# Optimization experiments

Hardware: AMD Instinct MI355X
Metric: run time of the kernel (lower is better)

## Reference

```python
import jax, jax.numpy as jnp
import numpy as np

N = 30000   # nodes
E = 600000  # edges
IN = 256    # in_channels
HID = 128   # 2*out_channels
OUT = 64    # out_channels


def setup_inputs() -> dict:
    key = jax.random.key(0)
    k = jax.random.split(key, 6)
    x = jax.random.normal(k[0], (N, IN), dtype=jnp.float32)
    edge_index = jax.random.randint(k[1], (2, E), 0, N, dtype=jnp.int64)
    W1 = jax.random.normal(k[2], (IN, HID), dtype=jnp.float32) * (1.0 / np.sqrt(IN))
    b1 = jnp.zeros((HID,), dtype=jnp.float32)
    W2 = jax.random.normal(k[3], (HID, OUT), dtype=jnp.float32) * (1.0 / np.sqrt(HID))
    b2 = jnp.zeros((OUT,), dtype=jnp.float32)
    return {"x": x, "edge_index": edge_index, "W1": W1, "b1": b1, "W2": W2, "b2": b2}


def _gcn_norm(edge_index, n_nodes):
    # PyG gcn_norm with add_self_loops=True, edge_weight=1
    loop = jnp.arange(n_nodes, dtype=edge_index.dtype)
    src = jnp.concatenate([edge_index[0], loop])
    dst = jnp.concatenate([edge_index[1], loop])
    deg = jax.ops.segment_sum(jnp.ones_like(dst, dtype=jnp.float32), dst,
                              num_segments=n_nodes)
    dinv = jnp.where(deg > 0, jax.lax.rsqrt(deg), 0.0)
    norm = dinv[src] * dinv[dst]  # [E+N]
    return src, dst, norm


def _gcn_conv(h, src, dst, norm, W, b, n_nodes):
    h = h @ W                              # [N, out] linear first (PyG order)
    msg = h[src] * norm[:, None]           # gather + per-edge scale, [E+N, out]
    out = jax.ops.segment_sum(msg, dst, num_segments=n_nodes)  # scatter-add
    return out + b


def reference(x, edge_index, W1, b1, W2, b2):
    n_nodes = x.shape[0]
    src, dst, norm = _gcn_norm(edge_index, n_nodes)
    h = _gcn_conv(x, src, dst, norm, W1, b1, n_nodes)
    h = jax.nn.relu(h)
    return _gcn_conv(h, src, dst, norm, W2, b2, n_nodes)
```

## Files before the change

### kernel.cpp

```cpp
#include <hip/hip_runtime.h>


#define GCN_IN 256
#define GCN_HID 128
#define GCN_OUT 64

#define BKT 128
#define SBE 4096
#define CAP 4096
#define SRCM 0x1FFFFFFu

typedef unsigned short ushort_t;
typedef __attribute__((ext_vector_type(8))) short short8;
typedef __attribute__((ext_vector_type(8))) unsigned short ushort8;
typedef __attribute__((ext_vector_type(4))) float f32x4;

__device__ inline float bf2f(ushort_t u) {
  union { unsigned int i; float f; } x; x.i = ((unsigned int)u) << 16; return x.f;
}
__device__ inline ushort_t f2bf(float f) {
  union { float f; unsigned int i; } u; u.f = f;
  unsigned int r = u.i + 0x7FFFu + ((u.i >> 16) & 1u);
  return (ushort_t)(r >> 16);
}

__global__ __launch_bounds__(256)
void stageX_kernel(const int* __restrict__ ei, int E,
                   int* __restrict__ gcur, int nbin,
                   unsigned int* __restrict__ stage) {
  __shared__ int lcnt[256];
  __shared__ int cur[256];
  __shared__ int nzc;
  const int t = threadIdx.x;
  const int sb = blockIdx.x;
  lcnt[t] = 0;
  if (t == 0) nzc = 0;
  __syncthreads();
  if (t < 128 && ei[2 * t + 1] != 0) atomicAdd(&nzc, 1);
  __syncthreads();
  const bool i64 = (nzc == 0);
  const int base = sb * SBE;
  int end = base + SBE; if (end > E) end = E;

  unsigned int p[16];
  int bk[16];
#pragma unroll
  for (int k = 0; k < 16; ++k) {
    int i = base + t + k * 256;
    bk[k] = -1;
    if (i < end) {
      int s, d;
      if (i64) { s = ei[2 * i]; d = ei[2 * E + 2 * i]; }
      else     { s = ei[i];     d = ei[E + i]; }
      p[k] = (unsigned int)s | ((unsigned int)(d & 127) << 25);
      bk[k] = d >> 7;
      atomicAdd(&lcnt[bk[k]], 1);
    }
  }
  __syncthreads();
  for (int b = t; b < nbin; b += 256) {
    int c = lcnt[b];
    cur[b] = b * CAP + (c ? atomicAdd(&gcur[b], c) : 0);
  }
  __syncthreads();
#pragma unroll
  for (int k = 0; k < 16; ++k) {
    if (bk[k] >= 0) {
      int pos = atomicAdd(&cur[bk[k]], 1);
      if (pos < (bk[k] + 1) * CAP)
        stage[pos] = p[k];
    }
  }
}

__global__ __launch_bounds__(256)
void scatter_kernel(const unsigned int* __restrict__ stage,
                    const int* __restrict__ gcur, int nbin,
                    int* __restrict__ csr_src,
                    int* __restrict__ row_ptr, int* __restrict__ deg,
                    float* __restrict__ dinv, int n) {
  __shared__ int lcnt[BKT];
  __shared__ int lscan[BKT];
  __shared__ int lcur[BKT];
  const int t = threadIdx.x;
  const int b = blockIdx.x;
  const int node0 = b * BKT;
  const int nn = (n - node0 < BKT) ? (n - node0) : BKT;
  const int rb = b * CAP;
  const int re = rb + gcur[b];
  if (t < BKT) lcnt[t] = 0;
  __syncthreads();
  for (int i = rb + t; i < re; i += 256)
    atomicAdd(&lcnt[stage[i] >> 25], 1);
  __syncthreads();
  if (t < BKT) lscan[t] = lcnt[t];
  __syncthreads();
  for (int off = 1; off < BKT; off <<= 1) {
    int v = 0;
    if (t < BKT && t >= off) v = lscan[t - off];
    __syncthreads();
    if (t < BKT) lscan[t] += v;
    __syncthreads();
  }
  if (t < BKT) {
    int excl = rb + lscan[t] - lcnt[t];
    lcur[t] = excl;
    if (t < nn) {
      row_ptr[node0 + t] = excl;
      deg[node0 + t] = lcnt[t];
      dinv[node0 + t] = rsqrtf((float)(lcnt[t] + 1));
    }
  }
  __syncthreads();
  for (int i = rb + t; i < re; i += 256) {
    unsigned int p = stage[i];
    int l = p >> 25;
    int pos = atomicAdd(&lcur[l], 1);
    csr_src[pos] = (int)(p & SRCM);
  }
}

__global__ void prep_w_kernel(const void* __restrict__ W1, const void* __restrict__ W2,
                              ushort_t* __restrict__ Wt1, ushort_t* __restrict__ Wt2,
                              int* __restrict__ flags, int* __restrict__ gcur) {
  __shared__ int csh;
  if (threadIdx.x == 0) csh = 0;
  __syncthreads();
  if (threadIdx.x < 128) {
    ushort_t u = ((const ushort_t*)W1)[2 * threadIdx.x];
    int e = (u >> 7) & 0xFF;
    if (e >= 100 && e <= 140) atomicAdd(&csh, 1);
  }
  __syncthreads();
  bool f32 = (csh < 64);
  if (blockIdx.x == 0) {
    if (threadIdx.x == 0) flags[0] = f32 ? 1 : 0;
    gcur[threadIdx.x] = 0;
  }

  int i = blockIdx.x * blockDim.x + threadIdx.x;
  if (i < GCN_IN * GCN_HID) {
    int k = i >> 7, n = i & 127;
    float v = f32 ? ((const float*)W1)[i] : bf2f(((const ushort_t*)W1)[i]);
    Wt1[n * GCN_IN + k] = f2bf(v);
  }
  int j = i - GCN_IN * GCN_HID;
  if (j >= 0 && j < GCN_HID * GCN_OUT) {
    int k = j >> 6, n = j & 63;
    float v = f32 ? ((const float*)W2)[j] : bf2f(((const ushort_t*)W2)[j]);
    Wt2[n * GCN_HID + k] = f2bf(v);
  }
}

template<int K, int NC, int A_MODE>
__global__ __launch_bounds__(256)
void gemm_mfma_kernel(const void* __restrict__ A, const ushort_t* __restrict__ Bt,
                      ushort_t* __restrict__ C, int M, const int* __restrict__ flags) {
  constexpr int KH = (K > 128) ? 128 : K;
  constexpr int KPC = KH / 8;
  constexpr int NT = NC / 32;
  __shared__ ushort_t As[32 * KH];
  __shared__ ushort_t Bs[NC * KH];
  const int tid = threadIdx.x;
  const int wv = tid >> 6;
  const int lane = tid & 63;
  const int ml = lane & 15;
  const int quad = lane >> 4;
  const int row0 = blockIdx.x * 32;
  const int mrow = (wv & 1) * 16 + ml;
  const int ncol0 = (wv >> 1) * (NC / 2);
  const bool aF32 = (A_MODE == 0) && (flags[0] != 0);
  f32x4 acc[NT] = {};

  for (int ch = 0; ch < K; ch += KH) {
    if (ch) __syncthreads();
    for (int c = tid; c < 32 * KPC; c += 256) {
      int r = c / KPC, cq = c % KPC;
      ushort8 o;
      if (row0 + r < M) {
        if (aF32) {
          const float* ap = (const float*)A + (size_t)(row0 + r) * K + ch + cq * 8;
          float4 f0 = *(const float4*)ap;
          float4 f1 = *(const float4*)(ap + 4);
          o[0] = f2bf(f0.x); o[1] = f2bf(f0.y); o[2] = f2bf(f0.z); o[3] = f2bf(f0.w);
          o[4] = f2bf(f1.x); o[5] = f2bf(f1.y); o[6] = f2bf(f1.z); o[7] = f2bf(f1.w);
        } else {
          o = *(const ushort8*)((const ushort_t*)A + (size_t)(row0 + r) * K + ch + cq * 8);
        }
      } else {
        o = (ushort8)0;
      }
      int byte = (cq * 16) ^ ((r & 7) << 4);
      *(ushort8*)((char*)As + r * (KH * 2) + byte) = o;
    }
    for (int c = tid; c < NC * KPC; c += 256) {
      int nr = c / KPC, cq = c % KPC;
      ushort8 o = *(const ushort8*)(Bt + (size_t)nr * K + ch + cq * 8);
      int byte = (cq * 16) ^ ((nr & 7) << 4);
      *(ushort8*)((char*)Bs + nr * (KH * 2) + byte) = o;
    }
    __syncthreads();
#pragma unroll
    for (int kt = 0; kt < KH; kt += 32) {
      int abyte = (kt * 2 + quad * 16) ^ ((mrow & 7) << 4);
      short8 af = *(const short8*)((const char*)As + mrow * (KH * 2) + abyte);
#pragma unroll
      for (int t = 0; t < NT; ++t) {
        int nr = ncol0 + t * 16 + ml;
        int bbyte = (kt * 2 + quad * 16) ^ ((nr & 7) << 4);
        short8 bf = *(const short8*)((const char*)Bs + nr * (KH * 2) + bbyte);
        acc[t] = __builtin_amdgcn_mfma_f32_16x16x32_bf16(af, bf, acc[t], 0, 0, 0);
      }
    }
  }

  const int orow = row0 + (wv & 1) * 16 + quad * 4;
#pragma unroll
  for (int t = 0; t < NT; ++t) {
    int col = ncol0 + t * 16 + ml;
#pragma unroll
    for (int r = 0; r < 4; ++r) {
      if (orow + r < M)
        C[(size_t)(orow + r) * NC + col] = f2bf(acc[t][r]);
    }
  }
}


__global__ void aggregate_relu_kernel(const ushort_t* __restrict__ h,
                                      const int* __restrict__ row_ptr,
                                      const int* __restrict__ deg,
                                      const int* __restrict__ csr_src,
                                      const float* __restrict__ dinv,
                                      const void* __restrict__ bias,
                                      ushort_t* __restrict__ outp, int n,
                                      const int* __restrict__ flags) {
  int wave = threadIdx.x >> 6;
  int lane = threadIdx.x & 63;
  int v = blockIdx.x * (blockDim.x >> 6) + wave;
  if (v >= n) return;
  const int q = lane & 15, g = lane >> 4;
  float acc[8] = {};
  int beg = row_ptr[v], end = beg + deg[v];
  for (int base = beg; base < end; base += 64) {
    int navail = end - base; if (navail > 64) navail = 64;
    int sv = 0; float dv = 0.f;
    if (base + lane < end) { sv = csr_src[base + lane]; dv = dinv[sv]; }
    for (int j = 0; j < navail; j += 16) {
      int e0 = j + g, e1 = j + 4 + g, e2 = j + 8 + g, e3 = j + 12 + g;
      int s0 = __shfl(sv, e0), s1 = __shfl(sv, e1);
      int s2 = __shfl(sv, e2), s3 = __shfl(sv, e3);
      float d0 = __shfl(dv, e0), d1 = __shfl(dv, e1);
      float d2 = __shfl(dv, e2), d3 = __shfl(dv, e3);
      ushort8 hv0 = *(const ushort8*)(h + (size_t)s0 * GCN_HID + q * 8);
      ushort8 hv1 = *(const ushort8*)(h + (size_t)s1 * GCN_HID + q * 8);
      ushort8 hv2 = *(const ushort8*)(h + (size_t)s2 * GCN_HID + q * 8);
      ushort8 hv3 = *(const ushort8*)(h + (size_t)s3 * GCN_HID + q * 8);
#pragma unroll
      for (int k = 0; k < 8; ++k) {
        acc[k] = fmaf(d0, bf2f(hv0[k]), acc[k]);
        acc[k] = fmaf(d1, bf2f(hv1[k]), acc[k]);
        acc[k] = fmaf(d2, bf2f(hv2[k]), acc[k]);
        acc[k] = fmaf(d3, bf2f(hv3[k]), acc[k]);
      }
    }
  }
#pragma unroll
  for (int k = 0; k < 8; ++k) {
    acc[k] += __shfl_xor(acc[k], 16);
    acc[k] += __shfl_xor(acc[k], 32);
  }
  if (g == 0) {
    float di = dinv[v];
    float sl = di * di;
    ushort8 hv = *(const ushort8*)(h + (size_t)v * GCN_HID + q * 8);
    const bool bF32 = flags[0] != 0;
    ushort8 o;
#pragma unroll
    for (int k = 0; k < 8; ++k) {
      float bv = bF32 ? ((const float*)bias)[q * 8 + k]
                      : bf2f(((const ushort_t*)bias)[q * 8 + k]);
      o[k] = f2bf(fmaxf(di * acc[k] + sl * bf2f(hv[k]) + bv, 0.f));
    }
    *(ushort8*)(outp + (size_t)v * GCN_HID + q * 8) = o;
  }
}

__global__ void aggregate_out_kernel(const ushort_t* __restrict__ h,
                                     const int* __restrict__ row_ptr,
                                     const int* __restrict__ deg,
                                     const int* __restrict__ csr_src,
                                     const float* __restrict__ dinv,
                                     const void* __restrict__ bias,
                                     void* __restrict__ outp, int n,
                                     const int* __restrict__ flags) {
  int wave = threadIdx.x >> 6;
  int lane = threadIdx.x & 63;
  int v = blockIdx.x * (blockDim.x >> 6) + wave;
  if (v >= n) return;
  const int q = lane & 7, g = lane >> 3;
  float acc[8] = {};
  int beg = row_ptr[v], end = beg + deg[v];
  for (int base = beg; base < end; base += 64) {
    int navail = end - base; if (navail > 64) navail = 64;
    int sv = 0; float dv = 0.f;
    if (base + lane < end) { sv = csr_src[base + lane]; dv = dinv[sv]; }
    for (int j = 0; j < navail; j += 32) {
      int e0 = j + g, e1 = j + 8 + g, e2 = j + 16 + g, e3 = j + 24 + g;
      int s0 = __shfl(sv, e0), s1 = __shfl(sv, e1);
      int s2 = __shfl(sv, e2), s3 = __shfl(sv, e3);
      float d0 = __shfl(dv, e0), d1 = __shfl(dv, e1);
      float d2 = __shfl(dv, e2), d3 = __shfl(dv, e3);
      ushort8 hv0 = *(const ushort8*)(h + (size_t)s0 * GCN_OUT + q * 8);
      ushort8 hv1 = *(const ushort8*)(h + (size_t)s1 * GCN_OUT + q * 8);
      ushort8 hv2 = *(const ushort8*)(h + (size_t)s2 * GCN_OUT + q * 8);
      ushort8 hv3 = *(const ushort8*)(h + (size_t)s3 * GCN_OUT + q * 8);
#pragma unroll
      for (int k = 0; k < 8; ++k) {
        acc[k] = fmaf(d0, bf2f(hv0[k]), acc[k]);
        acc[k] = fmaf(d1, bf2f(hv1[k]), acc[k]);
        acc[k] = fmaf(d2, bf2f(hv2[k]), acc[k]);
        acc[k] = fmaf(d3, bf2f(hv3[k]), acc[k]);
      }
    }
  }
#pragma unroll
  for (int k = 0; k < 8; ++k) {
    acc[k] += __shfl_xor(acc[k], 8);
    acc[k] += __shfl_xor(acc[k], 16);
    acc[k] += __shfl_xor(acc[k], 32);
  }
  if (g == 0) {
    float di = dinv[v];
    float sl = di * di;
    ushort8 hv = *(const ushort8*)(h + (size_t)v * GCN_OUT + q * 8);
    const bool oF32 = flags[0] != 0;
    float r[8];
#pragma unroll
    for (int k = 0; k < 8; ++k) {
      float bv = oF32 ? ((const float*)bias)[q * 8 + k]
                      : bf2f(((const ushort_t*)bias)[q * 8 + k]);
      r[k] = di * acc[k] + sl * bf2f(hv[k]) + bv;
    }
    if (oF32) {
      float* op = (float*)outp + (size_t)v * GCN_OUT + q * 8;
      *(float4*)op = make_float4(r[0], r[1], r[2], r[3]);
      *(float4*)(op + 4) = make_float4(r[4], r[5], r[6], r[7]);
    } else {
      ushort8 o;
#pragma unroll
      for (int k = 0; k < 8; ++k) o[k] = f2bf(r[k]);
      *(ushort8*)((ushort_t*)outp + (size_t)v * GCN_OUT + q * 8) = o;
    }
  }
}


extern "C" void kernel_launch(void* const* d_in, const int* in_sizes, int n_in,
                              void* d_out, int out_size, void* d_ws, size_t ws_size,
                              hipStream_t stream) {
  const void* x  = d_in[0];
  const int*  ei = (const int*)d_in[1];
  const void* W1 = d_in[2];
  const void* b1 = d_in[3];
  const void* W2 = d_in[4];
  const void* b2 = d_in[5];

  const int N = in_sizes[0] / GCN_IN;
  const int E = in_sizes[1] / 2;
  const int nsb  = (E + SBE - 1) / SBE;
  const int nbin = (N + BKT - 1) / BKT;

  size_t off = 0;
  auto alloc = [&](size_t bytes) -> void* {
    void* p = (char*)d_ws + off;
    off += (bytes + 255) & ~(size_t)255;
    return p;
  };
  int*          flags   = (int*)alloc(256);
  int*          gcur    = (int*)alloc(256 * 4);
  unsigned int* stage   = (unsigned int*)alloc((size_t)nbin * CAP * 4);
  int*          csr_src = (int*)alloc((size_t)nbin * CAP * 4);
  int*          row_ptr = (int*)alloc((size_t)N * 4);
  int*          deg     = (int*)alloc((size_t)N * 4);
  float*        dinv    = (float*)alloc((size_t)N * 4);
  ushort_t*     h1      = (ushort_t*)alloc((size_t)N * GCN_HID * 2);
  ushort_t*     hag     = (ushort_t*)alloc((size_t)N * GCN_HID * 2);
  ushort_t*     wt1     = (ushort_t*)alloc((size_t)GCN_HID * GCN_IN * 2);
  ushort_t*     wt2     = (ushort_t*)alloc((size_t)GCN_OUT * GCN_HID * 2);
  ushort_t*     h2      = h1;

  prep_w_kernel<<<(GCN_IN * GCN_HID + GCN_HID * GCN_OUT + 255) / 256, 256, 0, stream>>>(
      W1, W2, wt1, wt2, flags, gcur);

  stageX_kernel<<<nsb, 256, 0, stream>>>(ei, E, gcur, nbin, stage);
  scatter_kernel<<<nbin, 256, 0, stream>>>(stage, gcur, nbin, csr_src,
                                           row_ptr, deg, dinv, N);

  gemm_mfma_kernel<GCN_IN, GCN_HID, 0>
      <<<(N + 31) / 32, 256, 0, stream>>>(x, wt1, h1, N, flags);

  int gAgg = (N + 3) / 4;
  aggregate_relu_kernel<<<gAgg, 256, 0, stream>>>(h1, row_ptr, deg, csr_src,
                                                  dinv, b1, hag, N, flags);

  gemm_mfma_kernel<GCN_HID, GCN_OUT, 2>
      <<<(N + 31) / 32, 256, 0, stream>>>(hag, wt2, h2, N, flags);

  aggregate_out_kernel<<<gAgg, 256, 0, stream>>>(h2, row_ptr, deg, csr_src,
                                                 dinv, b2, d_out, N, flags);
}
```

Baseline: 160.8 us.

## Use fixed per-cell staging, fold weight prep into staging, narrow aggregation groups

Edge bucketing now writes into fixed-size cells indexed by (bin, superblock), so global atomics and the gcur reset go away. The weight transpose and dtype-detection kernel is folded into the staging kernel, which saves one launch. Both aggregation kernels now assign 16 or 8 lanes per node instead of a whole wave, which removes the cross-lane reductions and packs more nodes per block. Cells are capped at 64 edges, so an overflowing cell would silently drop edges. Per-node parallelism is also reduced for high-degree nodes.

```diff
diff --git a/kernel.cpp b/kernel.cpp
--- a/kernel.cpp
+++ b/kernel.cpp
@@ -7,7 +7,7 @@
 
 #define BKT 128
 #define SBE 4096
-#define CAP 4096
+#define CELL 64
 #define SRCM 0x1FFFFFFu
 
 typedef unsigned short ushort_t;
@@ -26,59 +26,67 @@
 
 __global__ __launch_bounds__(256)
 void stageX_kernel(const int* __restrict__ ei, int E,
-                   int* __restrict__ gcur, int nbin,
-                   unsigned int* __restrict__ stage) {
-  __shared__ int lcnt[256];
+                   const void* __restrict__ W1, const void* __restrict__ W2,
+                   ushort_t* __restrict__ Wt1, ushort_t* __restrict__ Wt2,
+                   int* __restrict__ flags, int nsb, int nbin,
+                   unsigned int* __restrict__ stage, int* __restrict__ cellcnt) {
   __shared__ int cur[256];
-  __shared__ int nzc;
+  __shared__ int nzc, csh;
   const int t = threadIdx.x;
   const int sb = blockIdx.x;
-  lcnt[t] = 0;
-  if (t == 0) nzc = 0;
-  __syncthreads();
-  if (t < 128 && ei[2 * t + 1] != 0) atomicAdd(&nzc, 1);
+  if (t == 0) { nzc = 0; csh = 0; }
+  __syncthreads();
+  if (t < 128) {
+    if (ei[2 * t + 1] != 0) atomicAdd(&nzc, 1);
+    ushort_t u = ((const ushort_t*)W1)[2 * t];
+    int e = (u >> 7) & 0xFF;
+    if (e >= 100 && e <= 140) atomicAdd(&csh, 1);
+  }
+  for (int b = t; b < nbin; b += 256) cur[b] = (b * nsb + sb) * CELL;
   __syncthreads();
   const bool i64 = (nzc == 0);
+  const bool f32 = (csh < 64);
+  if (sb == 0 && t == 0) flags[0] = f32 ? 1 : 0;
+
+  for (int i = sb * 256 + t; i < GCN_IN * GCN_HID + GCN_HID * GCN_OUT;
+       i += gridDim.x * 256) {
+    if (i < GCN_IN * GCN_HID) {
+      int k = i >> 7, nn = i & 127;
+      float vv = f32 ? ((const float*)W1)[i] : bf2f(((const ushort_t*)W1)[i]);
+      Wt1[nn * GCN_IN + k] = f2bf(vv);
+    } else {
+      int j = i - GCN_IN * GCN_HID;
+      int k = j >> 6, nn = j & 63;
+      float vv = f32 ? ((const float*)W2)[j] : bf2f(((const ushort_t*)W2)[j]);
+      Wt2[nn * GCN_HID + k] = f2bf(vv);
+    }
+  }
+
   const int base = sb * SBE;
   int end = base + SBE; if (end > E) end = E;
-
-  unsigned int p[16];
-  int bk[16];
-#pragma unroll
-  for (int k = 0; k < 16; ++k) {
-    int i = base + t + k * 256;
-    bk[k] = -1;
-    if (i < end) {
-      int s, d;
-      if (i64) { s = ei[2 * i]; d = ei[2 * E + 2 * i]; }
-      else     { s = ei[i];     d = ei[E + i]; }
-      p[k] = (unsigned int)s | ((unsigned int)(d & 127) << 25);
-      bk[k] = d >> 7;
-      atomicAdd(&lcnt[bk[k]], 1);
-    }
+  for (int i = base + t; i < end; i += 256) {
+    int s, d;
+    if (i64) { s = ei[2 * i]; d = ei[2 * E + 2 * i]; }
+    else     { s = ei[i];     d = ei[E + i]; }
+    int b = d >> 7;
+    int pos = atomicAdd(&cur[b], 1);
+    if (pos - (b * nsb + sb) * CELL < CELL)
+      stage[pos] = (unsigned int)s | ((unsigned int)(d & 127) << 25);
   }
   __syncthreads();
   for (int b = t; b < nbin; b += 256) {
-    int c = lcnt[b];
-    cur[b] = b * CAP + (c ? atomicAdd(&gcur[b], c) : 0);
-  }
-  __syncthreads();
-#pragma unroll
-  for (int k = 0; k < 16; ++k) {
-    if (bk[k] >= 0) {
-      int pos = atomicAdd(&cur[bk[k]], 1);
-      if (pos < (bk[k] + 1) * CAP)
-        stage[pos] = p[k];
-    }
+    int c = cur[b] - (b * nsb + sb) * CELL;
+    cellcnt[b * nsb + sb] = (c > CELL) ? CELL : c;
   }
 }
 
 __global__ __launch_bounds__(256)
 void scatter_kernel(const unsigned int* __restrict__ stage,
-                    const int* __restrict__ gcur, int nbin,
+                    const int* __restrict__ cellcnt, int nsb, int nbin,
                     int* __restrict__ csr_src,
                     int* __restrict__ row_ptr, int* __restrict__ deg,
                     float* __restrict__ dinv, int n) {
+  __shared__ int ccnt[256];
   __shared__ int lcnt[BKT];
   __shared__ int lscan[BKT];
   __shared__ int lcur[BKT];
@@ -86,12 +94,15 @@
   const int b = blockIdx.x;
   const int node0 = b * BKT;
   const int nn = (n - node0 < BKT) ? (n - node0) : BKT;
-  const int rb = b * CAP;
-  const int re = rb + gcur[b];
+  if (t < nsb) ccnt[t] = cellcnt[b * nsb + t];
   if (t < BKT) lcnt[t] = 0;
   __syncthreads();
-  for (int i = rb + t; i < re; i += 256)
-    atomicAdd(&lcnt[stage[i] >> 25], 1);
+  const unsigned int* srow = stage + (size_t)b * nsb * CELL;
+  const int tot = nsb * CELL;
+  for (int idx = t; idx < tot; idx += 256) {
+    if ((idx & (CELL - 1)) < ccnt[idx >> 6])
+      atomicAdd(&lcnt[srow[idx] >> 25], 1);
+  }
   __syncthreads();
   if (t < BKT) lscan[t] = lcnt[t];
   __syncthreads();
@@ -102,6 +113,7 @@
     if (t < BKT) lscan[t] += v;
     __syncthreads();
   }
+  const int rb = b * nsb * CELL;
   if (t < BKT) {
     int excl = rb + lscan[t] - lcnt[t];
     lcur[t] = excl;
@@ -112,43 +124,13 @@
     }
   }
   __syncthreads();
-  for (int i = rb + t; i < re; i += 256) {
-    unsigned int p = stage[i];
-    int l = p >> 25;
-    int pos = atomicAdd(&lcur[l], 1);
-    csr_src[pos] = (int)(p & SRCM);
-  }
-}
-
-__global__ void prep_w_kernel(const void* __restrict__ W1, const void* __restrict__ W2,
-                              ushort_t* __restrict__ Wt1, ushort_t* __restrict__ Wt2,
-                              int* __restrict__ flags, int* __restrict__ gcur) {
-  __shared__ int csh;
-  if (threadIdx.x == 0) csh = 0;
-  __syncthreads();
-  if (threadIdx.x < 128) {
-    ushort_t u = ((const ushort_t*)W1)[2 * threadIdx.x];
-    int e = (u >> 7) & 0xFF;
-    if (e >= 100 && e <= 140) atomicAdd(&csh, 1);
-  }
-  __syncthreads();
-  bool f32 = (csh < 64);
-  if (blockIdx.x == 0) {
-    if (threadIdx.x == 0) flags[0] = f32 ? 1 : 0;
-    gcur[threadIdx.x] = 0;
-  }
-
-  int i = blockIdx.x * blockDim.x + threadIdx.x;
-  if (i < GCN_IN * GCN_HID) {
-    int k = i >> 7, n = i & 127;
-    float v = f32 ? ((const float*)W1)[i] : bf2f(((const ushort_t*)W1)[i]);
-    Wt1[n * GCN_IN + k] = f2bf(v);
-  }
-  int j = i - GCN_IN * GCN_HID;
-  if (j >= 0 && j < GCN_HID * GCN_OUT) {
-    int k = j >> 6, n = j & 63;
-    float v = f32 ? ((const float*)W2)[j] : bf2f(((const ushort_t*)W2)[j]);
-    Wt2[n * GCN_HID + k] = f2bf(v);
+  for (int idx = t; idx < tot; idx += 256) {
+    if ((idx & (CELL - 1)) < ccnt[idx >> 6]) {
+      unsigned int p = srow[idx];
+      int l = p >> 25;
+      int pos = atomicAdd(&lcur[l], 1);
+      csr_src[pos] = (int)(p & SRCM);
+    }
   }
 }
 
@@ -226,7 +208,6 @@
   }
 }
 
-
 __global__ void aggregate_relu_kernel(const ushort_t* __restrict__ h,
                                       const int* __restrict__ row_ptr,
                                       const int* __restrict__ deg,
@@ -235,23 +216,23 @@
                                       const void* __restrict__ bias,
                                       ushort_t* __restrict__ outp, int n,
                                       const int* __restrict__ flags) {
-  int wave = threadIdx.x >> 6;
-  int lane = threadIdx.x & 63;
-  int v = blockIdx.x * (blockDim.x >> 6) + wave;
+  const int lane = threadIdx.x & 63;
+  const int v = blockIdx.x * 16 + (threadIdx.x >> 4);
   if (v >= n) return;
-  const int q = lane & 15, g = lane >> 4;
+  const int q = lane & 15;
+  const int gb = lane & 48;
   float acc[8] = {};
-  int beg = row_ptr[v], end = beg + deg[v];
-  for (int base = beg; base < end; base += 64) {
-    int navail = end - base; if (navail > 64) navail = 64;
+  const int beg = row_ptr[v];
+  const int end = beg + deg[v];
+  for (int base = beg; base < end; base += 16) {
+    int navail = end - base; if (navail > 16) navail = 16;
     int sv = 0; float dv = 0.f;
-    if (base + lane < end) { sv = csr_src[base + lane]; dv = dinv[sv]; }
-    for (int j = 0; j < navail; j += 16) {
-      int e0 = j + g, e1 = j + 4 + g, e2 = j + 8 + g, e3 = j + 12 + g;
-      int s0 = __shfl(sv, e0), s1 = __shfl(sv, e1);
-      int s2 = __shfl(sv, e2), s3 = __shfl(sv, e3);
-      float d0 = __shfl(dv, e0), d1 = __shfl(dv, e1);
-      float d2 = __shfl(dv, e2), d3 = __shfl(dv, e3);
+    if (base + q < end) { sv = csr_src[base + q]; dv = dinv[sv]; }
+    for (int j = 0; j < navail; j += 4) {
+      int s0 = __shfl(sv, gb + j + 0), s1 = __shfl(sv, gb + j + 1);
+      int s2 = __shfl(sv, gb + j + 2), s3 = __shfl(sv, gb + j + 3);
+      float d0 = __shfl(dv, gb + j + 0), d1 = __shfl(dv, gb + j + 1);
+      float d2 = __shfl(dv, gb + j + 2), d3 = __shfl(dv, gb + j + 3);
       ushort8 hv0 = *(const ushort8*)(h + (size_t)s0 * GCN_HID + q * 8);
       ushort8 hv1 = *(const ushort8*)(h + (size_t)s1 * GCN_HID + q * 8);
       ushort8 hv2 = *(const ushort8*)(h + (size_t)s2 * GCN_HID + q * 8);
@@ -265,25 +246,18 @@
       }
     }
   }
+  float di = dinv[v];
+  float sl = di * di;
+  ushort8 hv = *(const ushort8*)(h + (size_t)v * GCN_HID + q * 8);
+  const bool bF32 = flags[0] != 0;
+  ushort8 o;
 #pragma unroll
   for (int k = 0; k < 8; ++k) {
-    acc[k] += __shfl_xor(acc[k], 16);
-    acc[k] += __shfl_xor(acc[k], 32);
-  }
-  if (g == 0) {
-    float di = dinv[v];
-    float sl = di * di;
-    ushort8 hv = *(const ushort8*)(h + (size_t)v * GCN_HID + q * 8);
-    const bool bF32 = flags[0] != 0;
-    ushort8 o;
-#pragma unroll
-    for (int k = 0; k < 8; ++k) {
-      float bv = bF32 ? ((const float*)bias)[q * 8 + k]
-                      : bf2f(((const ushort_t*)bias)[q * 8 + k]);
-      o[k] = f2bf(fmaxf(di * acc[k] + sl * bf2f(hv[k]) + bv, 0.f));
-    }
-    *(ushort8*)(outp + (size_t)v * GCN_HID + q * 8) = o;
-  }
+    float bv = bF32 ? ((const float*)bias)[q * 8 + k]
+                    : bf2f(((const ushort_t*)bias)[q * 8 + k]);
+    o[k] = f2bf(fmaxf(di * acc[k] + sl * bf2f(hv[k]) + bv, 0.f));
+  }
+  *(ushort8*)(outp + (size_t)v * GCN_HID + q * 8) = o;
 }
 
 __global__ void aggregate_out_kernel(const ushort_t* __restrict__ h,
@@ -294,23 +268,23 @@
                                      const void* __restrict__ bias,
                                      void* __restrict__ outp, int n,
                                      const int* __restrict__ flags) {
-  int wave = threadIdx.x >> 6;
-  int lane = threadIdx.x & 63;
-  int v = blockIdx.x * (blockDim.x >> 6) + wave;
+  const int lane = threadIdx.x & 63;
+  const int v = blockIdx.x * 32 + (threadIdx.x >> 3);
   if (v >= n) return;
-  const int q = lane & 7, g = lane >> 3;
+  const int q = lane & 7;
+  const int gb = lane & 56;
   float acc[8] = {};
-  int beg = row_ptr[v], end = beg + deg[v];
-  for (int base = beg; base < end; base += 64) {
-    int navail = end - base; if (navail > 64) navail = 64;
+  const int beg = row_ptr[v];
+  const int end = beg + deg[v];
+  for (int base = beg; base < end; base += 8) {
+    int navail = end - base; if (navail > 8) navail = 8;
     int sv = 0; float dv = 0.f;
-    if (base + lane < end) { sv = csr_src[base + lane]; dv = dinv[sv]; }
-    for (int j = 0; j < navail; j += 32) {
-      int e0 = j + g, e1 = j + 8 + g, e2 = j + 16 + g, e3 = j + 24 + g;
-      int s0 = __shfl(sv, e0), s1 = __shfl(sv, e1);
-      int s2 = __shfl(sv, e2), s3 = __shfl(sv, e3);
-      float d0 = __shfl(dv, e0), d1 = __shfl(dv, e1);
-      float d2 = __shfl(dv, e2), d3 = __shfl(dv, e3);
+    if (base + q < end) { sv = csr_src[base + q]; dv = dinv[sv]; }
+    for (int j = 0; j < navail; j += 4) {
+      int s0 = __shfl(sv, gb + j + 0), s1 = __shfl(sv, gb + j + 1);
+      int s2 = __shfl(sv, gb + j + 2), s3 = __shfl(sv, gb + j + 3);
+      float d0 = __shfl(dv, gb + j + 0), d1 = __shfl(dv, gb + j + 1);
+      float d2 = __shfl(dv, gb + j + 2), d3 = __shfl(dv, gb + j + 3);
       ushort8 hv0 = *(const ushort8*)(h + (size_t)s0 * GCN_OUT + q * 8);
       ushort8 hv1 = *(const ushort8*)(h + (size_t)s1 * GCN_OUT + q * 8);
       ushort8 hv2 = *(const ushort8*)(h + (size_t)s2 * GCN_OUT + q * 8);
@@ -324,34 +298,26 @@
       }
     }
   }
+  float di = dinv[v];
+  float sl = di * di;
+  ushort8 hv = *(const ushort8*)(h + (size_t)v * GCN_OUT + q * 8);
+  const bool oF32 = flags[0] != 0;
+  float r[8];
 #pragma unroll
   for (int k = 0; k < 8; ++k) {
-    acc[k] += __shfl_xor(acc[k], 8);
-    acc[k] += __shfl_xor(acc[k], 16);
-    acc[k] += __shfl_xor(acc[k], 32);
-  }
-  if (g == 0) {
-    float di = dinv[v];
-    float sl = di * di;
-    ushort8 hv = *(const ushort8*)(h + (size_t)v * GCN_OUT + q * 8);
-    const bool oF32 = flags[0] != 0;
-    float r[8];
-#pragma unroll
-    for (int k = 0; k < 8; ++k) {
-      float bv = oF32 ? ((const float*)bias)[q * 8 + k]
-                      : bf2f(((const ushort_t*)bias)[q * 8 + k]);
-      r[k] = di * acc[k] + sl * bf2f(hv[k]) + bv;
-    }
-    if (oF32) {
-      float* op = (float*)outp + (size_t)v * GCN_OUT + q * 8;
-      *(float4*)op = make_float4(r[0], r[1], r[2], r[3]);
-      *(float4*)(op + 4) = make_float4(r[4], r[5], r[6], r[7]);
-    } else {
-      ushort8 o;
-#pragma unroll
-      for (int k = 0; k < 8; ++k) o[k] = f2bf(r[k]);
-      *(ushort8*)((ushort_t*)outp + (size_t)v * GCN_OUT + q * 8) = o;
-    }
+    float bv = oF32 ? ((const float*)bias)[q * 8 + k]
+                    : bf2f(((const ushort_t*)bias)[q * 8 + k]);
+    r[k] = di * acc[k] + sl * bf2f(hv[k]) + bv;
+  }
+  if (oF32) {
+    float* op = (float*)outp + (size_t)v * GCN_OUT + q * 8;
+    *(float4*)op = make_float4(r[0], r[1], r[2], r[3]);
+    *(float4*)(op + 4) = make_float4(r[4], r[5], r[6], r[7]);
+  } else {
+    ushort8 o;
+#pragma unroll
+    for (int k = 0; k < 8; ++k) o[k] = f2bf(r[k]);
+    *(ushort8*)((ushort_t*)outp + (size_t)v * GCN_OUT + q * 8) = o;
   }
 }
 
@@ -378,9 +344,9 @@
     return p;
   };
   int*          flags   = (int*)alloc(256);
-  int*          gcur    = (int*)alloc(256 * 4);
-  unsigned int* stage   = (unsigned int*)alloc((size_t)nbin * CAP * 4);
-  int*          csr_src = (int*)alloc((size_t)nbin * CAP * 4);
+  unsigned int* stage   = (unsigned int*)alloc((size_t)nbin * nsb * CELL * 4);
+  int*          cellcnt = (int*)alloc((size_t)nbin * nsb * 4);
+  int*          csr_src = (int*)alloc((size_t)nbin * nsb * CELL * 4);
   int*          row_ptr = (int*)alloc((size_t)N * 4);
   int*          deg     = (int*)alloc((size_t)N * 4);
   float*        dinv    = (float*)alloc((size_t)N * 4);
@@ -390,23 +356,20 @@
   ushort_t*     wt2     = (ushort_t*)alloc((size_t)GCN_OUT * GCN_HID * 2);
   ushort_t*     h2      = h1;
 
-  prep_w_kernel<<<(GCN_IN * GCN_HID + GCN_HID * GCN_OUT + 255) / 256, 256, 0, stream>>>(
-      W1, W2, wt1, wt2, flags, gcur);
-
-  stageX_kernel<<<nsb, 256, 0, stream>>>(ei, E, gcur, nbin, stage);
-  scatter_kernel<<<nbin, 256, 0, stream>>>(stage, gcur, nbin, csr_src,
+  stageX_kernel<<<nsb, 256, 0, stream>>>(ei, E, W1, W2, wt1, wt2, flags,
+                                         nsb, nbin, stage, cellcnt);
+  scatter_kernel<<<nbin, 256, 0, stream>>>(stage, cellcnt, nsb, nbin, csr_src,
                                            row_ptr, deg, dinv, N);
 
   gemm_mfma_kernel<GCN_IN, GCN_HID, 0>
       <<<(N + 31) / 32, 256, 0, stream>>>(x, wt1, h1, N, flags);
 
-  int gAgg = (N + 3) / 4;
-  aggregate_relu_kernel<<<gAgg, 256, 0, stream>>>(h1, row_ptr, deg, csr_src,
-                                                  dinv, b1, hag, N, flags);
+  aggregate_relu_kernel<<<(N + 15) / 16, 256, 0, stream>>>(
+      h1, row_ptr, deg, csr_src, dinv, b1, hag, N, flags);
 
   gemm_mfma_kernel<GCN_HID, GCN_OUT, 2>
       <<<(N + 31) / 32, 256, 0, stream>>>(hag, wt2, h2, N, flags);
 
-  aggregate_out_kernel<<<gAgg, 256, 0, stream>>>(h2, row_ptr, deg, csr_src,
-                                                 dinv, b2, d_out, N, flags);
-}
+  aggregate_out_kernel<<<(N + 31) / 32, 256, 0, stream>>>(
+      h2, row_ptr, deg, csr_src, dinv, b2, d_out, N, flags);
+}
```

Measured after the change: 171.9 us. 6.9% more time.
